# Performance work log

Measured on AMD Instinct MI355X. Metric: run time of the kernel, lower is better.

Reference implementation:

```python
import math
import jax, jax.numpy as jnp
import numpy as np

EMBED_DIM = 1024
NUM_HEADS = 16
HEAD_DIM = EMBED_DIM // NUM_HEADS


def setup_inputs() -> dict:
    key = jax.random.key(0)
    ks = jax.random.split(key, 10)
    B, S, E = 2, 2048, EMBED_DIM
    x = jax.random.normal(ks[0], (B, S, E), dtype=jnp.float32)
    mask = jax.random.randint(ks[1], (B, S), 0, 2, dtype=jnp.int32)
    s = 1.0 / math.sqrt(E)
    Wq = jax.random.normal(ks[2], (E, E), dtype=jnp.float32) * s
    bq = jnp.zeros((E,), dtype=jnp.float32)
    Wk = jax.random.normal(ks[3], (E, E), dtype=jnp.float32) * s
    bk = jnp.zeros((E,), dtype=jnp.float32)
    Wv = jax.random.normal(ks[4], (E, E), dtype=jnp.float32) * s
    bv = jnp.zeros((E,), dtype=jnp.float32)
    Wo = jax.random.normal(ks[5], (E, E), dtype=jnp.float32) * s
    bo = jnp.zeros((E,), dtype=jnp.float32)
    return {"x": x, "mask": mask, "Wq": Wq, "bq": bq, "Wk": Wk, "bk": bk,
            "Wv": Wv, "bv": bv, "Wo": Wo, "bo": bo}


def reference(x, mask, Wq, bq, Wk, bk, Wv, bv, Wo, bo):
    B, S, E = x.shape
    H, D = NUM_HEADS, HEAD_DIM
    scale = math.sqrt(D)  # ScaledDotProductAttention built with head_dim

    def split_heads(t):
        return t.reshape(B, S, H, D).transpose(0, 2, 1, 3)  # [B,H,S,D]

    q = split_heads(x @ Wq + bq)
    k = split_heads(x @ Wk + bk)
    v = split_heads(x @ Wv + bv)

    scores = jnp.einsum('bhqd,bhkd->bhqk', q, k) / scale  # [B,H,S,S]
    m = mask[:, None, None, :].astype(scores.dtype)        # [B,1,1,S]
    neg = jnp.finfo(scores.dtype).min
    scores = jnp.where(m == 0, neg, scores)
    aw = jax.nn.softmax(scores, axis=-1)
    # post-softmax mask renormalization (as in the torch module)
    aw = aw * m
    denom = aw.sum(axis=-1, keepdims=True)
    aw = jnp.where(denom > 0, aw / jnp.where(denom > 0, denom, 1.0), 0.0)

    ctx = jnp.einsum('bhqk,bhkd->bhqd', aw, v)             # [B,H,S,D]
    ctx = ctx.transpose(0, 2, 1, 3).reshape(B, S, E)
    out = ctx @ Wo + bo
    return out
```

## Files before the change

kernel.cpp:

```cpp
#include <hip/hip_runtime.h>

typedef _Float16 half8 __attribute__((ext_vector_type(8)));
typedef _Float16 half4v __attribute__((ext_vector_type(4)));
typedef _Float16 h2 __attribute__((ext_vector_type(2)));
typedef float f4 __attribute__((ext_vector_type(4)));

#define ASYNC_COPY16(ldsp, gp)                                                     \
  __builtin_amdgcn_global_load_lds((__attribute__((address_space(1))) void*)(gp),  \
                                   (__attribute__((address_space(3))) void*)(ldsp),\
                                   16, 0, 0)

__device__ __forceinline__ f4 mfma16(half8 a, half8 b, f4 c) {
  return __builtin_amdgcn_mfma_f32_16x16x32_f16(a, b, c, 0, 0, 0);
}

__device__ __forceinline__ h2 pack2(float a, float b) {
  return __builtin_bit_cast(h2, __builtin_amdgcn_cvt_pkrtz(a, b));
}

#if defined(__has_builtin)
#if __has_builtin(__builtin_amdgcn_exp2f)
#define EXP2(x) __builtin_amdgcn_exp2f(x)
#endif
#if __has_builtin(__builtin_amdgcn_fdot2)
#define FDOT2(a, b, c) __builtin_amdgcn_fdot2((a), (b), (c), false)
#endif
#endif
#ifndef EXP2
#define EXP2(x) __expf((x) * 0.69314718056f)
#endif
#define KSCALE 0.18033688011f
#define FIXMAX 10.0f


__global__ __launch_bounds__(256) void k_prep(
    const float* __restrict__ x, _Float16* __restrict__ xh,
    const float* __restrict__ Wq, const float* __restrict__ Wk,
    const float* __restrict__ Wv, const float* __restrict__ Wo,
    _Float16* __restrict__ wqkvT, _Float16* __restrict__ woT) {
  __shared__ float tw[32][33];
  const int bid = blockIdx.x, t = threadIdx.x;
  if (bid < 4096) {
    int i = (bid * 256 + t) * 4;
    f4 v = *(const f4*)(x + i);
    half4v h;
    h[0] = (_Float16)v[0]; h[1] = (_Float16)v[1];
    h[2] = (_Float16)v[2]; h[3] = (_Float16)v[3];
    *(half4v*)(xh + i) = h;
    return;
  }
  const int idx = bid - 4096;
  const int z = idx >> 10, rem = idx & 1023;
  const int n0 = (rem & 31) * 32, k0 = (rem >> 5) * 32;
  const float* w = (z == 0) ? Wq : (z == 1) ? Wk : (z == 2) ? Wv : Wo;
  _Float16* wt = (z == 3) ? woT : wqkvT + (size_t)z * 1048576;
  const int tx = t & 31, ty = t >> 5;
  for (int j = 0; j < 32; j += 8) tw[ty + j][tx] = w[(size_t)(k0 + ty + j) * 1024 + n0 + tx];
  __syncthreads();
  for (int j = 0; j < 32; j += 8)
    wt[(size_t)(n0 + ty + j) * 1024 + k0 + tx] = (_Float16)tw[tx][ty + j];
}

__global__ __launch_bounds__(256) void k_gemm_proj(
    const _Float16* __restrict__ A, const _Float16* __restrict__ Bt,
    const float* __restrict__ bq, const float* __restrict__ bk, const float* __restrict__ bv,
    _Float16* __restrict__ Qo, _Float16* __restrict__ Ko, _Float16* __restrict__ Vto) {
  __shared__ __align__(16) _Float16 As[128 * 32];
  __shared__ __align__(16) _Float16 Bs[128 * 32];
  const int t = threadIdx.x, lane = t & 63, w = t >> 6;
  const int qd = lane >> 4, lr = lane & 15;
  const int m0 = blockIdx.y * 128, n0 = blockIdx.x * 128;
  const int wm = (w & 1) * 64, wn = (w >> 1) * 64;
  const f4 z4 = {0.f, 0.f, 0.f, 0.f};
  f4 acc[4][4];
#pragma unroll
  for (int i = 0; i < 4; ++i)
#pragma unroll
    for (int j = 0; j < 4; ++j) acc[i][j] = z4;

  const int c0 = t, c1 = t + 256;
  for (int k0 = 0; k0 < 1024; k0 += 32) {
    const _Float16* ga0 = A + (size_t)(m0 + (c0 >> 2)) * 1024 + k0 + (c0 & 3) * 8;
    const _Float16* ga1 = A + (size_t)(m0 + (c1 >> 2)) * 1024 + k0 + (c1 & 3) * 8;
    const _Float16* gb0 = Bt + (size_t)(n0 + (c0 >> 2)) * 1024 + k0 + (c0 & 3) * 8;
    const _Float16* gb1 = Bt + (size_t)(n0 + (c1 >> 2)) * 1024 + k0 + (c1 & 3) * 8;
    char* la = (char*)As + w * 1024;
    char* lb = (char*)Bs + w * 1024;
    ASYNC_COPY16(la, ga0);
    ASYNC_COPY16(la + 4096, ga1);
    ASYNC_COPY16(lb, gb0);
    ASYNC_COPY16(lb + 4096, gb1);
    __syncthreads();
    half8 af[4], bf[4];
#pragma unroll
    for (int i = 0; i < 4; ++i)
      af[i] = *(const half8*)(As + (wm + i * 16 + lr) * 32 + qd * 8);
#pragma unroll
    for (int j = 0; j < 4; ++j)
      bf[j] = *(const half8*)(Bs + (wn + j * 16 + lr) * 32 + qd * 8);
#pragma unroll
    for (int i = 0; i < 4; ++i)
#pragma unroll
      for (int j = 0; j < 4; ++j) acc[i][j] = mfma16(af[i], bf[j], acc[i][j]);
    __syncthreads();
  }

  const int mat = n0 >> 10;
  const float* bias = (mat == 0) ? bq : (mat == 1) ? bk : bv;
  if (mat == 2) {
#pragma unroll
    for (int i = 0; i < 4; ++i)
#pragma unroll
      for (int j = 0; j < 4; ++j) {
        int n = (n0 + wn + j * 16 + lr) & 1023;
        int hh = n >> 6, d = n & 63;
        int mb = m0 + wm + i * 16 + qd * 4;
        int bb = mb >> 11, sb = mb & 2047;
        float bval = bias[n];
        half4v hv;
#pragma unroll
        for (int r = 0; r < 4; ++r) hv[r] = (_Float16)(acc[i][j][r] + bval);
        *(half4v*)(Vto + ((size_t)(bb * 16 + hh) * 64 + d) * 2048 + sb) = hv;
      }
  } else {
    _Float16* outp = (mat == 0) ? Qo : Ko;
    const float scl = (mat == 0) ? KSCALE : 1.f;
#pragma unroll
    for (int i = 0; i < 4; ++i)
#pragma unroll
      for (int j = 0; j < 4; ++j)
#pragma unroll
        for (int r = 0; r < 4; ++r) {
          int m = m0 + wm + i * 16 + qd * 4 + r;
          int n = (n0 + wn + j * 16 + lr) & 1023;
          float v = (acc[i][j][r] + bias[n]) * scl;
          int bb = m >> 11, s = m & 2047, hh = n >> 6, d = n & 63;
          outp[(size_t)((bb * 16 + hh) * 2048 + s) * 64 + d] = (_Float16)v;
        }
  }
}

__global__ __launch_bounds__(256, 2) void k_attn(
    const _Float16* __restrict__ Qg, const _Float16* __restrict__ Kg,
    const _Float16* __restrict__ Vtg, const int* __restrict__ maskg,
    _Float16* __restrict__ Op, float* __restrict__ ml) {
  __shared__ __align__(16) _Float16 Ks[64][72];
  __shared__ __align__(16) _Float16 Vts[64][72];
  __shared__ __align__(16) _Float16 Pq[4][16][72];
  __shared__ float Msk[64];

  const int bh = blockIdx.y;
  const int b = bh >> 4;
  const int q0 = blockIdx.x * 256;
  const int z = blockIdx.z;
  const int kb = z * 1024;
  const int t = threadIdx.x, lane = t & 63, w = t >> 6;
  const int qd = lane >> 4, lr = lane & 15;

  half8 qf[4][2];
#pragma unroll
  for (int rt = 0; rt < 4; ++rt)
#pragma unroll
    for (int ks = 0; ks < 2; ++ks)
      qf[rt][ks] = *(const half8*)(Qg + (size_t)(bh * 2048 + q0 + w * 64 + rt * 16 + lr) * 64 +
                                   ks * 32 + qd * 8);

  float l_i[4] = {0.f, 0.f, 0.f, 0.f};
  const f4 z4 = {0.f, 0.f, 0.f, 0.f};
  f4 O[4][4];
#pragma unroll
  for (int rt = 0; rt < 4; ++rt)
#pragma unroll
    for (int dt = 0; dt < 4; ++dt) O[rt][dt] = z4;

  const int sr0 = t >> 3, scc = (t & 7) * 8;
  const int sr1 = sr0 + 32;
  const _Float16* Kbase = Kg + (size_t)bh * 2048 * 64 + (size_t)kb * 64;
  const _Float16* Vtbase = Vtg + (size_t)bh * 64 * 2048 + kb;

  f4 kr0 = *(const f4*)(Kbase + (size_t)sr0 * 64 + scc);
  f4 kr1 = *(const f4*)(Kbase + (size_t)sr1 * 64 + scc);
  f4 vr0 = *(const f4*)(Vtbase + (size_t)sr0 * 2048 + scc);
  f4 vr1 = *(const f4*)(Vtbase + (size_t)sr1 * 2048 + scc);
  float mval = 0.f;
  if (t < 64) mval = maskg[b * 2048 + kb + t] ? -FIXMAX : -30010.f;

#if defined(FDOT2)
  const h2 one2 = {(_Float16)1.f, (_Float16)1.f};
#endif

  for (int it = 0; it < 16; ++it) {
    __syncthreads();
    *(f4*)&Ks[sr0][scc] = kr0;
    *(f4*)&Ks[sr1][scc] = kr1;
    *(f4*)&Vts[sr0][scc] = vr0;
    *(f4*)&Vts[sr1][scc] = vr1;
    if (t < 64) Msk[t] = mval;
    __syncthreads();

    if (it < 15) {
      int kk = (it + 1) * 64;
      kr0 = *(const f4*)(Kbase + (size_t)(kk + sr0) * 64 + scc);
      kr1 = *(const f4*)(Kbase + (size_t)(kk + sr1) * 64 + scc);
      vr0 = *(const f4*)(Vtbase + (size_t)sr0 * 2048 + kk + scc);
      vr1 = *(const f4*)(Vtbase + (size_t)sr1 * 2048 + kk + scc);
      if (t < 64) mval = maskg[b * 2048 + kb + kk + t] ? -FIXMAX : -30010.f;
    }

    half8 bp[4][2];
#pragma unroll
    for (int rtp = 0; rtp < 2; ++rtp) {
      const int r0 = rtp * 2, r1 = rtp * 2 + 1;
      f4 sc[2][4];
#pragma unroll
      for (int kt = 0; kt < 4; ++kt) {
        f4 mv = *(const f4*)&Msk[kt * 16 + qd * 4];
        sc[0][kt] = mv;
        sc[1][kt] = mv;
      }
      __builtin_amdgcn_s_setprio(1);
#pragma unroll
      for (int kt = 0; kt < 4; ++kt) {
        half8 k0 = *(const half8*)&Ks[kt * 16 + lr][qd * 8];
        half8 k1 = *(const half8*)&Ks[kt * 16 + lr][32 + qd * 8];
        sc[0][kt] = mfma16(k0, qf[r0][0], sc[0][kt]);
        sc[0][kt] = mfma16(k1, qf[r0][1], sc[0][kt]);
        sc[1][kt] = mfma16(k0, qf[r1][0], sc[1][kt]);
        sc[1][kt] = mfma16(k1, qf[r1][1], sc[1][kt]);
      }
      __builtin_amdgcn_s_setprio(0);

#pragma unroll
      for (int rr = 0; rr < 2; ++rr) {
        const int rt = rtp * 2 + rr;
        float s = 0.f;
#pragma unroll
        for (int kt = 0; kt < 4; ++kt) {
          float p0 = EXP2(sc[rr][kt][0]);
          float p1 = EXP2(sc[rr][kt][1]);
          float p2 = EXP2(sc[rr][kt][2]);
          float p3 = EXP2(sc[rr][kt][3]);
          h2 pa = pack2(p0, p1);
          h2 pb = pack2(p2, p3);
#if defined(FDOT2)
          s = FDOT2(pa, one2, s);
          s = FDOT2(pb, one2, s);
#else
          s += p0 + p1 + p2 + p3;
#endif
          half4v hv;
          hv.lo = pa;
          hv.hi = pb;
          *(half4v*)&Pq[w][lr][kt * 16 + qd * 4] = hv;
        }
        s += __shfl_xor(s, 16, 64);
        s += __shfl_xor(s, 32, 64);
        l_i[rt] += s;

        bp[rt][0] = *(const half8*)&Pq[w][lr][qd * 8];
        bp[rt][1] = *(const half8*)&Pq[w][lr][32 + qd * 8];
      }
    }

    __builtin_amdgcn_s_setprio(1);
#pragma unroll
    for (int dt = 0; dt < 4; ++dt) {
      half8 va0 = *(const half8*)&Vts[dt * 16 + lr][qd * 8];
      half8 va1 = *(const half8*)&Vts[dt * 16 + lr][32 + qd * 8];
#pragma unroll
      for (int rt = 0; rt < 4; ++rt) {
        O[rt][dt] = mfma16(va0, bp[rt][0], O[rt][dt]);
        O[rt][dt] = mfma16(va1, bp[rt][1], O[rt][dt]);
      }
    }
    __builtin_amdgcn_s_setprio(0);
  }

#pragma unroll
  for (int rt = 0; rt < 4; ++rt) {
    int qrow = q0 + w * 64 + rt * 16 + lr;
    size_t rowi = (size_t)(z * 32 + bh) * 2048 + qrow;
    _Float16* op = Op + rowi * 64;
#pragma unroll
    for (int dt = 0; dt < 4; ++dt) {
      half4v hv;
#pragma unroll
      for (int r = 0; r < 4; ++r) hv[r] = (_Float16)O[rt][dt][r];
      *(half4v*)(op + dt * 16 + qd * 4) = hv;
    }
    if (qd == 0) ml[rowi] = l_i[rt];
  }
}

__global__ __launch_bounds__(256) void k_merge(const _Float16* __restrict__ Op,
                                               const float* __restrict__ ml,
                                               _Float16* __restrict__ ctx) {
  int idx = blockIdx.x * 256 + threadIdx.x;
  int d8 = (idx & 7) * 8;
  int h = (idx >> 3) & 15;
  int q = idx >> 7;
  int b = q >> 11, s = q & 2047;
  int bh = b * 16 + h;
  size_t r1 = (size_t)bh * 2048 + s;
  size_t r2 = (size_t)(32 + bh) * 2048 + s;
  float l1 = ml[r1], l2 = ml[r2];
  float inv = 1.f / fmaxf(l1 + l2, 1e-20f);
  half8 o1 = *(const half8*)(Op + r1 * 64 + d8);
  half8 o2 = *(const half8*)(Op + r2 * 64 + d8);
  half8 ho;
#pragma unroll
  for (int j = 0; j < 8; ++j)
    ho[j] = (_Float16)(((float)o1[j] + (float)o2[j]) * inv);
  *(half8*)(ctx + (size_t)q * 1024 + h * 64 + d8) = ho;
}

__global__ __launch_bounds__(256) void k_gemm_out(
    const _Float16* __restrict__ A, const _Float16* __restrict__ Bt,
    const float* __restrict__ bo, float* __restrict__ out) {
  __shared__ __align__(16) _Float16 As[64 * 32];
  __shared__ __align__(16) _Float16 Bs[128 * 32];
  const int t = threadIdx.x, lane = t & 63, w = t >> 6;
  const int qd = lane >> 4, lr = lane & 15;
  const int m0 = blockIdx.y * 64, n0 = blockIdx.x * 128;
  const int wm = (w & 1) * 32, wn = (w >> 1) * 64;
  const f4 z4 = {0.f, 0.f, 0.f, 0.f};
  f4 acc[2][4];
#pragma unroll
  for (int i = 0; i < 2; ++i)
#pragma unroll
    for (int j = 0; j < 4; ++j) acc[i][j] = z4;

  const int c0 = t, c1 = t + 256;
  for (int k0 = 0; k0 < 1024; k0 += 32) {
    const _Float16* ga = A + (size_t)(m0 + (t >> 2)) * 1024 + k0 + (t & 3) * 8;
    const _Float16* gb0 = Bt + (size_t)(n0 + (c0 >> 2)) * 1024 + k0 + (c0 & 3) * 8;
    const _Float16* gb1 = Bt + (size_t)(n0 + (c1 >> 2)) * 1024 + k0 + (c1 & 3) * 8;
    char* la = (char*)As + w * 1024;
    char* lb = (char*)Bs + w * 1024;
    ASYNC_COPY16(la, ga);
    ASYNC_COPY16(lb, gb0);
    ASYNC_COPY16(lb + 4096, gb1);
    __syncthreads();
    half8 af[2], bf[4];
#pragma unroll
    for (int i = 0; i < 2; ++i)
      af[i] = *(const half8*)(As + (wm + i * 16 + lr) * 32 + qd * 8);
#pragma unroll
    for (int j = 0; j < 4; ++j)
      bf[j] = *(const half8*)(Bs + (wn + j * 16 + lr) * 32 + qd * 8);
#pragma unroll
    for (int i = 0; i < 2; ++i)
#pragma unroll
      for (int j = 0; j < 4; ++j) acc[i][j] = mfma16(af[i], bf[j], acc[i][j]);
    __syncthreads();
  }
#pragma unroll
  for (int i = 0; i < 2; ++i)
#pragma unroll
    for (int j = 0; j < 4; ++j)
#pragma unroll
      for (int r = 0; r < 4; ++r) {
        int m = m0 + wm + i * 16 + qd * 4 + r;
        int n = n0 + wn + j * 16 + lr;
        out[(size_t)m * 1024 + n] = acc[i][j][r] + bo[n];
      }
}

extern "C" void kernel_launch(void* const* d_in, const int* in_sizes, int n_in,
                              void* d_out, int out_size, void* d_ws, size_t ws_size,
                              hipStream_t stream) {
  const float* x = (const float*)d_in[0];
  const int* mask = (const int*)d_in[1];
  const float* Wq = (const float*)d_in[2];
  const float* bq = (const float*)d_in[3];
  const float* Wk = (const float*)d_in[4];
  const float* bk = (const float*)d_in[5];
  const float* Wv = (const float*)d_in[6];
  const float* bv = (const float*)d_in[7];
  const float* Wo = (const float*)d_in[8];
  const float* bo = (const float*)d_in[9];
  float* out = (float*)d_out;
  char* ws = (char*)d_ws;
  const size_t MB = 1 << 20;

  _Float16* Oph   = (_Float16*)(ws + 0);
  _Float16* xh    = (_Float16*)(ws + 0);
  _Float16* wqkvT = (_Float16*)(ws + 8 * MB);
  _Float16* woT   = (_Float16*)(ws + 16 * MB);
  _Float16* Qh    = (_Float16*)(ws + 18 * MB);
  _Float16* ctxh  = (_Float16*)(ws + 18 * MB);
  _Float16* Kh    = (_Float16*)(ws + 26 * MB);
  _Float16* Vth   = (_Float16*)(ws + 34 * MB);
  float*    mlw   = (float*)   (ws + 42 * MB);

  k_prep<<<dim3(8192), dim3(256), 0, stream>>>(x, xh, Wq, Wk, Wv, Wo, wqkvT, woT);
  k_gemm_proj<<<dim3(24, 32), dim3(256), 0, stream>>>(xh, wqkvT, bq, bk, bv, Qh, Kh, Vth);
  k_attn<<<dim3(8, 32, 2), dim3(256), 0, stream>>>(Qh, Kh, Vth, mask, Oph, mlw);
  k_merge<<<dim3(2048), dim3(256), 0, stream>>>(Oph, mlw, ctxh);
  k_gemm_out<<<dim3(8, 64), dim3(256), 0, stream>>>(ctxh, woT, bo, out);
}
```

Before: 202.4 us.

## Halve attention query tile and compute row sums with MFMA against ones

Each attention block now handles 128 query rows instead of 256, so twice as many blocks launch and the occupancy hint rises from 2 to 3 blocks per CU. The per-row softmax denominators are no longer summed with fdot2 and cross-lane shuffles. They come from an extra MFMA of a ones vector against the packed probability fragments, which reuses the matrix unit instead of VALU work. In exchange, the K/V tiles are loaded into LDS twice as often per query row, and the matrix unit does a little more work per tile.

```diff
diff --git a/kernel.cpp b/kernel.cpp
--- a/kernel.cpp
+++ b/kernel.cpp
@@ -21,9 +21,6 @@
 #if defined(__has_builtin)
 #if __has_builtin(__builtin_amdgcn_exp2f)
 #define EXP2(x) __builtin_amdgcn_exp2f(x)
-#endif
-#if __has_builtin(__builtin_amdgcn_fdot2)
-#define FDOT2(a, b, c) __builtin_amdgcn_fdot2((a), (b), (c), false)
 #endif
 #endif
 #ifndef EXP2
@@ -140,7 +137,7 @@
   }
 }
 
-__global__ __launch_bounds__(256, 2) void k_attn(
+__global__ __launch_bounds__(256, 3) void k_attn(
     const _Float16* __restrict__ Qg, const _Float16* __restrict__ Kg,
     const _Float16* __restrict__ Vtg, const int* __restrict__ maskg,
     _Float16* __restrict__ Op, float* __restrict__ ml) {
@@ -151,27 +148,32 @@
 
   const int bh = blockIdx.y;
   const int b = bh >> 4;
-  const int q0 = blockIdx.x * 256;
+  const int q0 = blockIdx.x * 128;
   const int z = blockIdx.z;
   const int kb = z * 1024;
   const int t = threadIdx.x, lane = t & 63, w = t >> 6;
   const int qd = lane >> 4, lr = lane & 15;
 
-  half8 qf[4][2];
-#pragma unroll
-  for (int rt = 0; rt < 4; ++rt)
+  half8 qf[2][2];
+#pragma unroll
+  for (int rt = 0; rt < 2; ++rt)
 #pragma unroll
     for (int ks = 0; ks < 2; ++ks)
-      qf[rt][ks] = *(const half8*)(Qg + (size_t)(bh * 2048 + q0 + w * 64 + rt * 16 + lr) * 64 +
+      qf[rt][ks] = *(const half8*)(Qg + (size_t)(bh * 2048 + q0 + w * 32 + rt * 16 + lr) * 64 +
                                    ks * 32 + qd * 8);
 
-  float l_i[4] = {0.f, 0.f, 0.f, 0.f};
   const f4 z4 = {0.f, 0.f, 0.f, 0.f};
-  f4 O[4][4];
-#pragma unroll
-  for (int rt = 0; rt < 4; ++rt)
+  f4 O[2][4];
+  f4 Ol[2];
+#pragma unroll
+  for (int rt = 0; rt < 2; ++rt) {
+    Ol[rt] = z4;
 #pragma unroll
     for (int dt = 0; dt < 4; ++dt) O[rt][dt] = z4;
+  }
+  half8 ones8;
+#pragma unroll
+  for (int j = 0; j < 8; ++j) ones8[j] = (_Float16)1.f;
 
   const int sr0 = t >> 3, scc = (t & 7) * 8;
   const int sr1 = sr0 + 32;
@@ -184,10 +186,6 @@
   f4 vr1 = *(const f4*)(Vtbase + (size_t)sr1 * 2048 + scc);
   float mval = 0.f;
   if (t < 64) mval = maskg[b * 2048 + kb + t] ? -FIXMAX : -30010.f;
-
-#if defined(FDOT2)
-  const h2 one2 = {(_Float16)1.f, (_Float16)1.f};
-#endif
 
   for (int it = 0; it < 16; ++it) {
     __syncthreads();
@@ -207,59 +205,41 @@
       if (t < 64) mval = maskg[b * 2048 + kb + kk + t] ? -FIXMAX : -30010.f;
     }
 
-    half8 bp[4][2];
-#pragma unroll
-    for (int rtp = 0; rtp < 2; ++rtp) {
-      const int r0 = rtp * 2, r1 = rtp * 2 + 1;
-      f4 sc[2][4];
+    f4 sc[2][4];
+#pragma unroll
+    for (int kt = 0; kt < 4; ++kt) {
+      f4 mv = *(const f4*)&Msk[kt * 16 + qd * 4];
+      sc[0][kt] = mv;
+      sc[1][kt] = mv;
+    }
+    __builtin_amdgcn_s_setprio(1);
+#pragma unroll
+    for (int kt = 0; kt < 4; ++kt) {
+      half8 k0 = *(const half8*)&Ks[kt * 16 + lr][qd * 8];
+      half8 k1 = *(const half8*)&Ks[kt * 16 + lr][32 + qd * 8];
+      sc[0][kt] = mfma16(k0, qf[0][0], sc[0][kt]);
+      sc[0][kt] = mfma16(k1, qf[0][1], sc[0][kt]);
+      sc[1][kt] = mfma16(k0, qf[1][0], sc[1][kt]);
+      sc[1][kt] = mfma16(k1, qf[1][1], sc[1][kt]);
+    }
+    __builtin_amdgcn_s_setprio(0);
+
+    half8 bp[2][2];
+#pragma unroll
+    for (int rt = 0; rt < 2; ++rt) {
 #pragma unroll
       for (int kt = 0; kt < 4; ++kt) {
-        f4 mv = *(const f4*)&Msk[kt * 16 + qd * 4];
-        sc[0][kt] = mv;
-        sc[1][kt] = mv;
+        float p0 = EXP2(sc[rt][kt][0]);
+        float p1 = EXP2(sc[rt][kt][1]);
+        float p2 = EXP2(sc[rt][kt][2]);
+        float p3 = EXP2(sc[rt][kt][3]);
+        half4v hv;
+        hv.lo = pack2(p0, p1);
+        hv.hi = pack2(p2, p3);
+        *(half4v*)&Pq[w][lr][kt * 16 + qd * 4] = hv;
       }
-      __builtin_amdgcn_s_setprio(1);
-#pragma unroll
-      for (int kt = 0; kt < 4; ++kt) {
-        half8 k0 = *(const half8*)&Ks[kt * 16 + lr][qd * 8];
-        half8 k1 = *(const half8*)&Ks[kt * 16 + lr][32 + qd * 8];
-        sc[0][kt] = mfma16(k0, qf[r0][0], sc[0][kt]);
-        sc[0][kt] = mfma16(k1, qf[r0][1], sc[0][kt]);
-        sc[1][kt] = mfma16(k0, qf[r1][0], sc[1][kt]);
-        sc[1][kt] = mfma16(k1, qf[r1][1], sc[1][kt]);
-      }
-      __builtin_amdgcn_s_setprio(0);
-
-#pragma unroll
-      for (int rr = 0; rr < 2; ++rr) {
-        const int rt = rtp * 2 + rr;
-        float s = 0.f;
-#pragma unroll
-        for (int kt = 0; kt < 4; ++kt) {
-          float p0 = EXP2(sc[rr][kt][0]);
-          float p1 = EXP2(sc[rr][kt][1]);
-          float p2 = EXP2(sc[rr][kt][2]);
-          float p3 = EXP2(sc[rr][kt][3]);
-          h2 pa = pack2(p0, p1);
-          h2 pb = pack2(p2, p3);
-#if defined(FDOT2)
-          s = FDOT2(pa, one2, s);
-          s = FDOT2(pb, one2, s);
-#else
-          s += p0 + p1 + p2 + p3;
-#endif
-          half4v hv;
-          hv.lo = pa;
-          hv.hi = pb;
-          *(half4v*)&Pq[w][lr][kt * 16 + qd * 4] = hv;
-        }
-        s += __shfl_xor(s, 16, 64);
-        s += __shfl_xor(s, 32, 64);
-        l_i[rt] += s;
-
-        bp[rt][0] = *(const half8*)&Pq[w][lr][qd * 8];
-        bp[rt][1] = *(const half8*)&Pq[w][lr][32 + qd * 8];
-      }
+      bp[rt][0] = *(const half8*)&Pq[w][lr][qd * 8];
+      bp[rt][1] = *(const half8*)&Pq[w][lr][32 + qd * 8];
     }
 
     __builtin_amdgcn_s_setprio(1);
@@ -268,17 +248,22 @@
       half8 va0 = *(const half8*)&Vts[dt * 16 + lr][qd * 8];
       half8 va1 = *(const half8*)&Vts[dt * 16 + lr][32 + qd * 8];
 #pragma unroll
-      for (int rt = 0; rt < 4; ++rt) {
+      for (int rt = 0; rt < 2; ++rt) {
         O[rt][dt] = mfma16(va0, bp[rt][0], O[rt][dt]);
         O[rt][dt] = mfma16(va1, bp[rt][1], O[rt][dt]);
       }
     }
+#pragma unroll
+    for (int rt = 0; rt < 2; ++rt) {
+      Ol[rt] = mfma16(ones8, bp[rt][0], Ol[rt]);
+      Ol[rt] = mfma16(ones8, bp[rt][1], Ol[rt]);
+    }
     __builtin_amdgcn_s_setprio(0);
   }
 
 #pragma unroll
-  for (int rt = 0; rt < 4; ++rt) {
-    int qrow = q0 + w * 64 + rt * 16 + lr;
+  for (int rt = 0; rt < 2; ++rt) {
+    int qrow = q0 + w * 32 + rt * 16 + lr;
     size_t rowi = (size_t)(z * 32 + bh) * 2048 + qrow;
     _Float16* op = Op + rowi * 64;
 #pragma unroll
@@ -288,7 +273,7 @@
       for (int r = 0; r < 4; ++r) hv[r] = (_Float16)O[rt][dt][r];
       *(half4v*)(op + dt * 16 + qd * 4) = hv;
     }
-    if (qd == 0) ml[rowi] = l_i[rt];
+    if (qd == 0) ml[rowi] = Ol[rt][0];
   }
 }
 
@@ -395,7 +380,7 @@
 
   k_prep<<<dim3(8192), dim3(256), 0, stream>>>(x, xh, Wq, Wk, Wv, Wo, wqkvT, woT);
   k_gemm_proj<<<dim3(24, 32), dim3(256), 0, stream>>>(xh, wqkvT, bq, bk, bv, Qh, Kh, Vth);
-  k_attn<<<dim3(8, 32, 2), dim3(256), 0, stream>>>(Qh, Kh, Vth, mask, Oph, mlw);
+  k_attn<<<dim3(16, 32, 2), dim3(256), 0, stream>>>(Qh, Kh, Vth, mask, Oph, mlw);
   k_merge<<<dim3(2048), dim3(256), 0, stream>>>(Oph, mlw, ctxh);
   k_gemm_out<<<dim3(8, 64), dim3(256), 0, stream>>>(ctxh, woT, bo, out);
 }
```

After: 203.1 us. About the same (+0.3%).

## Compute softmax row sums via MFMA with ones, hoist K fragments, widen GEMM K-tile

Applied to the files above, without the earlier changes.

The attention kernel drops the per-row fdot2 accumulation and cross-lane shuffles. It computes the row sum of P by running extra MFMAs against a vector of ones, in the same way it accumulates P·V. K fragments are now loaded from LDS once per iteration instead of once per row-tile pair. The projection GEMM doubles its K tile from 32 to 64, which halves the number of barriers per output tile. The costs are eight extra MFMAs per iteration, more registers held for the K fragments, and twice the LDS used by the GEMM.

```diff
diff --git a/kernel.cpp b/kernel.cpp
--- a/kernel.cpp
+++ b/kernel.cpp
@@ -21,9 +21,6 @@
 #if defined(__has_builtin)
 #if __has_builtin(__builtin_amdgcn_exp2f)
 #define EXP2(x) __builtin_amdgcn_exp2f(x)
-#endif
-#if __has_builtin(__builtin_amdgcn_fdot2)
-#define FDOT2(a, b, c) __builtin_amdgcn_fdot2((a), (b), (c), false)
 #endif
 #endif
 #ifndef EXP2
@@ -65,8 +62,8 @@
     const _Float16* __restrict__ A, const _Float16* __restrict__ Bt,
     const float* __restrict__ bq, const float* __restrict__ bk, const float* __restrict__ bv,
     _Float16* __restrict__ Qo, _Float16* __restrict__ Ko, _Float16* __restrict__ Vto) {
-  __shared__ __align__(16) _Float16 As[128 * 32];
-  __shared__ __align__(16) _Float16 Bs[128 * 32];
+  __shared__ __align__(16) _Float16 As[128 * 64];
+  __shared__ __align__(16) _Float16 Bs[128 * 64];
   const int t = threadIdx.x, lane = t & 63, w = t >> 6;
   const int qd = lane >> 4, lr = lane & 15;
   const int m0 = blockIdx.y * 128, n0 = blockIdx.x * 128;
@@ -78,30 +75,31 @@
 #pragma unroll
     for (int j = 0; j < 4; ++j) acc[i][j] = z4;
 
-  const int c0 = t, c1 = t + 256;
-  for (int k0 = 0; k0 < 1024; k0 += 32) {
-    const _Float16* ga0 = A + (size_t)(m0 + (c0 >> 2)) * 1024 + k0 + (c0 & 3) * 8;
-    const _Float16* ga1 = A + (size_t)(m0 + (c1 >> 2)) * 1024 + k0 + (c1 & 3) * 8;
-    const _Float16* gb0 = Bt + (size_t)(n0 + (c0 >> 2)) * 1024 + k0 + (c0 & 3) * 8;
-    const _Float16* gb1 = Bt + (size_t)(n0 + (c1 >> 2)) * 1024 + k0 + (c1 & 3) * 8;
-    char* la = (char*)As + w * 1024;
-    char* lb = (char*)Bs + w * 1024;
-    ASYNC_COPY16(la, ga0);
-    ASYNC_COPY16(la + 4096, ga1);
-    ASYNC_COPY16(lb, gb0);
-    ASYNC_COPY16(lb + 4096, gb1);
-    __syncthreads();
-    half8 af[4], bf[4];
-#pragma unroll
-    for (int i = 0; i < 4; ++i)
-      af[i] = *(const half8*)(As + (wm + i * 16 + lr) * 32 + qd * 8);
-#pragma unroll
-    for (int j = 0; j < 4; ++j)
-      bf[j] = *(const half8*)(Bs + (wn + j * 16 + lr) * 32 + qd * 8);
-#pragma unroll
-    for (int i = 0; i < 4; ++i)
-#pragma unroll
-      for (int j = 0; j < 4; ++j) acc[i][j] = mfma16(af[i], bf[j], acc[i][j]);
+  const int sr = t >> 3;
+  const int sc8 = (t & 7) * 8;
+  for (int k0 = 0; k0 < 1024; k0 += 64) {
+#pragma unroll
+    for (int c = 0; c < 4; ++c) {
+      const _Float16* ga = A + (size_t)(m0 + c * 32 + sr) * 1024 + k0 + sc8;
+      const _Float16* gb = Bt + (size_t)(n0 + c * 32 + sr) * 1024 + k0 + sc8;
+      ASYNC_COPY16((char*)As + c * 4096 + w * 1024, ga);
+      ASYNC_COPY16((char*)Bs + c * 4096 + w * 1024, gb);
+    }
+    __syncthreads();
+#pragma unroll
+    for (int ks = 0; ks < 2; ++ks) {
+      half8 af[4], bf[4];
+#pragma unroll
+      for (int i = 0; i < 4; ++i)
+        af[i] = *(const half8*)(As + (wm + i * 16 + lr) * 64 + ks * 32 + qd * 8);
+#pragma unroll
+      for (int j = 0; j < 4; ++j)
+        bf[j] = *(const half8*)(Bs + (wn + j * 16 + lr) * 64 + ks * 32 + qd * 8);
+#pragma unroll
+      for (int i = 0; i < 4; ++i)
+#pragma unroll
+        for (int j = 0; j < 4; ++j) acc[i][j] = mfma16(af[i], bf[j], acc[i][j]);
+    }
     __syncthreads();
   }
 
@@ -165,13 +163,18 @@
       qf[rt][ks] = *(const half8*)(Qg + (size_t)(bh * 2048 + q0 + w * 64 + rt * 16 + lr) * 64 +
                                    ks * 32 + qd * 8);
 
-  float l_i[4] = {0.f, 0.f, 0.f, 0.f};
   const f4 z4 = {0.f, 0.f, 0.f, 0.f};
   f4 O[4][4];
-#pragma unroll
-  for (int rt = 0; rt < 4; ++rt)
+  f4 Ol[4];
+#pragma unroll
+  for (int rt = 0; rt < 4; ++rt) {
+    Ol[rt] = z4;
 #pragma unroll
     for (int dt = 0; dt < 4; ++dt) O[rt][dt] = z4;
+  }
+  half8 ones8;
+#pragma unroll
+  for (int j = 0; j < 8; ++j) ones8[j] = (_Float16)1.f;
 
   const int sr0 = t >> 3, scc = (t & 7) * 8;
   const int sr1 = sr0 + 32;
@@ -184,10 +187,6 @@
   f4 vr1 = *(const f4*)(Vtbase + (size_t)sr1 * 2048 + scc);
   float mval = 0.f;
   if (t < 64) mval = maskg[b * 2048 + kb + t] ? -FIXMAX : -30010.f;
-
-#if defined(FDOT2)
-  const h2 one2 = {(_Float16)1.f, (_Float16)1.f};
-#endif
 
   for (int it = 0; it < 16; ++it) {
     __syncthreads();
@@ -207,6 +206,13 @@
       if (t < 64) mval = maskg[b * 2048 + kb + kk + t] ? -FIXMAX : -30010.f;
     }
 
+    half8 kf0[4], kf1[4];
+#pragma unroll
+    for (int kt = 0; kt < 4; ++kt) {
+      kf0[kt] = *(const half8*)&Ks[kt * 16 + lr][qd * 8];
+      kf1[kt] = *(const half8*)&Ks[kt * 16 + lr][32 + qd * 8];
+    }
+
     half8 bp[4][2];
 #pragma unroll
     for (int rtp = 0; rtp < 2; ++rtp) {
@@ -221,42 +227,27 @@
       __builtin_amdgcn_s_setprio(1);
 #pragma unroll
       for (int kt = 0; kt < 4; ++kt) {
-        half8 k0 = *(const half8*)&Ks[kt * 16 + lr][qd * 8];
-        half8 k1 = *(const half8*)&Ks[kt * 16 + lr][32 + qd * 8];
-        sc[0][kt] = mfma16(k0, qf[r0][0], sc[0][kt]);
-        sc[0][kt] = mfma16(k1, qf[r0][1], sc[0][kt]);
-        sc[1][kt] = mfma16(k0, qf[r1][0], sc[1][kt]);
-        sc[1][kt] = mfma16(k1, qf[r1][1], sc[1][kt]);
+        sc[0][kt] = mfma16(kf0[kt], qf[r0][0], sc[0][kt]);
+        sc[0][kt] = mfma16(kf1[kt], qf[r0][1], sc[0][kt]);
+        sc[1][kt] = mfma16(kf0[kt], qf[r1][0], sc[1][kt]);
+        sc[1][kt] = mfma16(kf1[kt], qf[r1][1], sc[1][kt]);
       }
       __builtin_amdgcn_s_setprio(0);
 
 #pragma unroll
       for (int rr = 0; rr < 2; ++rr) {
         const int rt = rtp * 2 + rr;
-        float s = 0.f;
 #pragma unroll
         for (int kt = 0; kt < 4; ++kt) {
           float p0 = EXP2(sc[rr][kt][0]);
           float p1 = EXP2(sc[rr][kt][1]);
           float p2 = EXP2(sc[rr][kt][2]);
           float p3 = EXP2(sc[rr][kt][3]);
-          h2 pa = pack2(p0, p1);
-          h2 pb = pack2(p2, p3);
-#if defined(FDOT2)
-          s = FDOT2(pa, one2, s);
-          s = FDOT2(pb, one2, s);
-#else
-          s += p0 + p1 + p2 + p3;
-#endif
           half4v hv;
-          hv.lo = pa;
-          hv.hi = pb;
+          hv.lo = pack2(p0, p1);
+          hv.hi = pack2(p2, p3);
           *(half4v*)&Pq[w][lr][kt * 16 + qd * 4] = hv;
         }
-        s += __shfl_xor(s, 16, 64);
-        s += __shfl_xor(s, 32, 64);
-        l_i[rt] += s;
-
         bp[rt][0] = *(const half8*)&Pq[w][lr][qd * 8];
         bp[rt][1] = *(const half8*)&Pq[w][lr][32 + qd * 8];
       }
@@ -272,6 +263,11 @@
         O[rt][dt] = mfma16(va0, bp[rt][0], O[rt][dt]);
         O[rt][dt] = mfma16(va1, bp[rt][1], O[rt][dt]);
       }
+    }
+#pragma unroll
+    for (int rt = 0; rt < 4; ++rt) {
+      Ol[rt] = mfma16(ones8, bp[rt][0], Ol[rt]);
+      Ol[rt] = mfma16(ones8, bp[rt][1], Ol[rt]);
     }
     __builtin_amdgcn_s_setprio(0);
   }
@@ -288,7 +284,7 @@
       for (int r = 0; r < 4; ++r) hv[r] = (_Float16)O[rt][dt][r];
       *(half4v*)(op + dt * 16 + qd * 4) = hv;
     }
-    if (qd == 0) ml[rowi] = l_i[rt];
+    if (qd == 0) ml[rowi] = Ol[rt][0];
   }
 }
 
```

Result: slower. 213.5 us (+5.5%).
